# Kernel optimization log

Measured on AMD Instinct MI355X. Metric: run time of the kernel, lower is better.

## Reference

```python
import jax, jax.numpy as jnp
import numpy as np

N = 50000      # nodes
E = 600000     # edges (avg degree 12)
F_IN = 128     # num_features
H = 128        # hidden_feats (== F_IN so both conv layers share weight shapes)
C = 10         # num_classes
L = 2          # num_layers


def setup_inputs() -> dict:
    key = jax.random.key(0)
    ks = jax.random.split(key, 12)
    s = 0.05
    x = jax.random.normal(ks[0], (N, F_IN), dtype=jnp.float32)
    edge_index = jax.random.randint(ks[1], (2, E), 0, N, dtype=jnp.int64)
    # Stacked per-layer TransformerConv params (heads=1): query/key/value/skip linears.
    Wq = jax.random.normal(ks[2], (L, H, F_IN), dtype=jnp.float32) * s
    bq = jax.random.normal(ks[3], (L, H), dtype=jnp.float32) * s
    Wk = jax.random.normal(ks[4], (L, H, F_IN), dtype=jnp.float32) * s
    bk = jax.random.normal(ks[5], (L, H), dtype=jnp.float32) * s
    Wv = jax.random.normal(ks[6], (L, H, F_IN), dtype=jnp.float32) * s
    bv = jax.random.normal(ks[7], (L, H), dtype=jnp.float32) * s
    Ws = jax.random.normal(ks[8], (L, H, F_IN), dtype=jnp.float32) * s
    bs = jax.random.normal(ks[9], (L, H), dtype=jnp.float32) * s
    fc_W = jax.random.normal(ks[10], (C, H), dtype=jnp.float32) * s
    fc_b = jax.random.normal(ks[11], (C,), dtype=jnp.float32) * s
    return {"x": x, "edge_index": edge_index, "Wq": Wq, "bq": bq, "Wk": Wk,
            "bk": bk, "Wv": Wv, "bv": bv, "Ws": Ws, "bs": bs,
            "fc_W": fc_W, "fc_b": fc_b}


def _transformer_conv(h, src, dst, Wq, bq, Wk, bk, Wv, bv, Ws, bs):
    # PyG TransformerConv, heads=1, concat=True, root_weight=True, eval mode.
    d = Wq.shape[0]
    scale = 1.0 / np.sqrt(d).astype(np.float32)
    q = h @ Wq.T + bq          # [N, d]
    k = h @ Wk.T + bk          # [N, d]
    v = h @ Wv.T + bv          # [N, d]
    # per-edge attention score: <q_dst, k_src> / sqrt(d)
    scores = jnp.sum(q[dst] * k[src], axis=-1) * scale   # [E]
    # scatter-softmax over incoming edges of each destination node
    m = jax.ops.segment_max(scores, dst, num_segments=N)           # [N]
    e = jnp.exp(scores - m[dst])                                   # [E]
    denom = jax.ops.segment_sum(e, dst, num_segments=N)            # [N]
    alpha = e / denom[dst]                                         # [E]
    agg = jax.ops.segment_sum(alpha[:, None] * v[src], dst, num_segments=N)  # [N, d]
    return agg + (h @ Ws.T + bs)  # root/skip connection


def reference(x, edge_index, Wq, bq, Wk, bk, Wv, bv, Ws, bs, fc_W, fc_b):
    src = edge_index[0]
    dst = edge_index[1]
    h = x
    for l in range(L):  # fixed small layer loop
        h = _transformer_conv(h, src, dst, Wq[l], bq[l], Wk[l], bk[l],
                              Wv[l], bv[l], Ws[l], bs[l])
        h = jax.nn.relu(h)  # dropout is identity in eval mode
    logits = h @ fc_W.T + fc_b  # [N, C]
    return jax.nn.log_softmax(logits, axis=1)
```

## Files before the change

### kernel.cpp

```cpp
#include <hip/hip_runtime.h>
#include <math.h>

#define N_NODES 50000
#define N_EDGES 600000
#define DIM 128
#define NCLS 10
#define MTILES 391
#define CHUNKS_PER_TILE 2048
#define NB_SCAN 49

typedef __attribute__((ext_vector_type(8))) short short8b;
typedef __attribute__((ext_vector_type(4))) float f32x4;

__device__ inline unsigned short f2b(float f) {
    unsigned u = __float_as_uint(f);
    return (unsigned short)((u + 0x7FFFu + ((u >> 16) & 1u)) >> 16);
}
__device__ inline float b2f(unsigned short u) {
    return __uint_as_float(((unsigned)u) << 16);
}

__global__ void deg_kernel(const int* __restrict__ dst, int* __restrict__ deg) {
    int e = blockIdx.x * blockDim.x + threadIdx.x;
    if (e < N_EDGES) atomicAdd(&deg[dst[e]], 1);
}

__global__ __launch_bounds__(1024) void scan1_kernel(
        const int* __restrict__ deg, int* __restrict__ row_start,
        int* __restrict__ partials) {
    __shared__ int buf[1024];
    int b = blockIdx.x, t = threadIdx.x;
    int i = b * 1024 + t;
    buf[t] = (i < N_NODES) ? deg[i] : 0;
    __syncthreads();
    for (int off = 1; off < 1024; off <<= 1) {
        int tv = (t >= off) ? buf[t - off] : 0;
        __syncthreads();
        buf[t] += tv;
        __syncthreads();
    }
    if (i < N_NODES) row_start[i + 1] = buf[t];
    if (t == 1023) partials[b] = buf[1023];
}

__global__ void scan2_kernel(const int* __restrict__ partials, int* __restrict__ blockoff) {
    if (threadIdx.x == 0) {
        int off = 0;
        for (int b = 0; b < NB_SCAN; ++b) { blockoff[b] = off; off += partials[b]; }
    }
}

__global__ __launch_bounds__(1024) void scan3_kernel(
        const int* __restrict__ blockoff, int* __restrict__ row_start) {
    int b = blockIdx.x, t = threadIdx.x;
    int i = b * 1024 + t;
    if (i < N_NODES) row_start[i + 1] += blockoff[b];
    if (i == 0) row_start[0] = 0;
}

__global__ void fill_kernel(const int* __restrict__ src, const int* __restrict__ dst,
                            const int* __restrict__ row_start, int* __restrict__ cursor,
                            int* __restrict__ col) {
    int e = blockIdx.x * blockDim.x + threadIdx.x;
    if (e < N_EDGES) {
        int d = dst[e];
        int pos = atomicAdd(&cursor[d], 1);
        col[row_start[d] + pos] = src[e];
    }
}

__global__ __launch_bounds__(256) void wfrag_kernel(
        const float* __restrict__ Wq, const float* __restrict__ Wk,
        const float* __restrict__ Wv, const float* __restrict__ Ws,
        short* __restrict__ wfrag) {
    int mat = blockIdx.x;
    int l = mat >> 2, m = mat & 3;
    const float* W = (m == 0 ? Wq : m == 1 ? Wk : m == 2 ? Wv : Ws) + l * DIM * DIM;
    short* out = wfrag + (size_t)mat * (CHUNKS_PER_TILE * 8);
    for (int i = threadIdx.x; i < CHUNKS_PER_TILE; i += 256) {
        int tile = i >> 6, lane = i & 63;
        int row = (tile >> 2) * 16 + (lane & 15);
        int k0 = (tile & 3) * 32 + (lane >> 4) * 8;
        const float4* p = (const float4*)(W + row * DIM + k0);
        float4 a = p[0], b = p[1];
        short tmp[8];
        tmp[0] = (short)f2b(a.x); tmp[1] = (short)f2b(a.y);
        tmp[2] = (short)f2b(a.z); tmp[3] = (short)f2b(a.w);
        tmp[4] = (short)f2b(b.x); tmp[5] = (short)f2b(b.y);
        tmp[6] = (short)f2b(b.z); tmp[7] = (short)f2b(b.w);
        *(short8b*)(out + (size_t)i * 8) = *(short8b*)tmp;
    }
}

__global__ __launch_bounds__(256) void xb_kernel(const float* __restrict__ x,
                                                 unsigned short* __restrict__ xb) {
    int i = blockIdx.x * 256 + threadIdx.x;
    if (i >= N_NODES * DIM / 8) return;
    const float4* p = (const float4*)(x + (size_t)i * 8);
    float4 a = p[0], b = p[1];
    unsigned short tmp[8];
    tmp[0] = f2b(a.x); tmp[1] = f2b(a.y); tmp[2] = f2b(a.z); tmp[3] = f2b(a.w);
    tmp[4] = f2b(b.x); tmp[5] = f2b(b.y); tmp[6] = f2b(b.z); tmp[7] = f2b(b.w);
    *(short8b*)(xb + (size_t)i * 8) = *(short8b*)tmp;
}

__global__ __launch_bounds__(512) void linear_kernel(
        const unsigned short* __restrict__ hb,
        const short* __restrict__ wfrag,
        const float* __restrict__ bq, const float* __restrict__ bk,
        const float* __restrict__ bv, const float* __restrict__ bs,
        unsigned short* __restrict__ Qb, unsigned short* __restrict__ Kb,
        unsigned short* __restrict__ Vb, unsigned short* __restrict__ Sb) {
    __shared__ short hs[16384];
    __shared__ short wsm[16384];
    int tid = threadIdx.x;
    int tile = blockIdx.x;
    short8b* lh = (short8b*)hs;
    short8b* lw = (short8b*)wsm;
    #pragma unroll
    for (int j = 0; j < 4; ++j) {
        int i = tid + j * 512;
        int s = i >> 6, lane = i & 63;
        int row = tile * 128 + ((s >> 2) << 4) + (lane & 15);
        int k0 = ((s & 3) << 5) + ((lane >> 4) << 3);
        row = row < N_NODES ? row : N_NODES - 1;
        lh[i] = *(const short8b*)((const short*)hb + (size_t)row * DIM + k0);
    }
    int wave = tid >> 6, lane = tid & 63;
    int colg = lane & 15, rowg = lane >> 4;

    for (int m = 0; m < 4; ++m) {
        const short8b* gw = (const short8b*)(wfrag + (size_t)m * (CHUNKS_PER_TILE * 8));
        __syncthreads();
        #pragma unroll
        for (int j = 0; j < 4; ++j) lw[tid + j * 512] = gw[tid + j * 512];
        __syncthreads();

        f32x4 acc[8];
        #pragma unroll
        for (int nt = 0; nt < 8; ++nt) acc[nt] = (f32x4){0.f, 0.f, 0.f, 0.f};
        #pragma unroll
        for (int ks = 0; ks < 4; ++ks) {
            short8b a = lh[(wave * 4 + ks) * 64 + lane];
            #pragma unroll
            for (int nt = 0; nt < 8; ++nt)
                acc[nt] = __builtin_amdgcn_mfma_f32_16x16x32_bf16(
                              a, lw[(nt * 4 + ks) * 64 + lane], acc[nt], 0, 0, 0);
        }

        const float* bias = (m == 0 ? bq : m == 1 ? bk : m == 2 ? bv : bs);
        unsigned short* out = (m == 0 ? Qb : m == 1 ? Kb : m == 2 ? Vb : Sb);
        int rowbase = tile * 128 + wave * 16 + rowg * 4;
        #pragma unroll
        for (int nt = 0; nt < 8; ++nt) {
            int colv = nt * 16 + colg;
            float bvv = bias[colv];
            #pragma unroll
            for (int r = 0; r < 4; ++r) {
                int row = rowbase + r;
                if (row < N_NODES)
                    out[(size_t)row * DIM + colv] = f2b(acc[nt][r] + bvv);
            }
        }
    }
}

__global__ __launch_bounds__(256) void attn_kernel(
        const unsigned short* __restrict__ Qb, const unsigned short* __restrict__ Kb,
        const unsigned short* __restrict__ Vb, const unsigned short* __restrict__ Sb,
        const int* __restrict__ row_start, const int* __restrict__ col,
        unsigned short* __restrict__ hout) {
    int wave = threadIdx.x >> 6;
    int lane = threadIdx.x & 63;
    int g = lane >> 4, gl = lane & 15;
    int n = blockIdx.x * 4 + wave;
    if (n >= N_NODES) return;

    short8b qu = *(const short8b*)((const short*)Qb + (size_t)n * DIM + gl * 8);
    float qf[8];
    #pragma unroll
    for (int j = 0; j < 8; ++j) qf[j] = b2f((unsigned short)qu[j]);

    int e0 = row_start[n], e1 = row_start[n + 1];
    const float NEG = -1.0e30f;
    float m = NEG, den = 0.f;
    float acc[8];
    #pragma unroll
    for (int j = 0; j < 8; ++j) acc[j] = 0.f;
    const float scale = 0.08838834764831843f;

    for (int eb = e0; eb < e1; eb += 4) {
        int e = eb + g;
        bool valid = e < e1;
        int s = col[valid ? e : e1 - 1];
        const short* base = (const short*)Kb + (size_t)s * DIM + gl * 8;
        short8b kv = *(const short8b*)base;
        short8b vv = *(const short8b*)((const short*)Vb + (size_t)s * DIM + gl * 8);
        float p = 0.f;
        #pragma unroll
        for (int j = 0; j < 8; ++j) p = fmaf(qf[j], b2f((unsigned short)kv[j]), p);
        p += __shfl_xor(p, 1);
        p += __shfl_xor(p, 2);
        p += __shfl_xor(p, 4);
        p += __shfl_xor(p, 8);
        p = valid ? p * scale : NEG;
        float nm = fmaxf(m, p);
        float fac = __expf(m - nm);
        float w = valid ? __expf(p - nm) : 0.f;
        den = den * fac + w;
        #pragma unroll
        for (int j = 0; j < 8; ++j)
            acc[j] = fmaf(acc[j], fac, w * b2f((unsigned short)vv[j]));
        m = nm;
    }

    float M = m;
    M = fmaxf(M, __shfl_xor(M, 16));
    M = fmaxf(M, __shfl_xor(M, 32));
    float fac = __expf(m - M);
    float d = den * fac;
    d += __shfl_xor(d, 16);
    d += __shfl_xor(d, 32);
    #pragma unroll
    for (int j = 0; j < 8; ++j) {
        float a = acc[j] * fac;
        a += __shfl_xor(a, 16);
        a += __shfl_xor(a, 32);
        acc[j] = a;
    }
    float inv = (d > 0.f) ? 1.f / d : 0.f;

    short8b su = *(const short8b*)((const short*)Sb + (size_t)n * DIM + gl * 8);
    short8b o;
    #pragma unroll
    for (int j = 0; j < 8; ++j)
        o[j] = (short)f2b(fmaxf(fmaf(acc[j], inv, b2f((unsigned short)su[j])), 0.f));
    if (g == 0)
        *(short8b*)((short*)hout + (size_t)n * DIM + gl * 8) = o;
}

__global__ __launch_bounds__(256) void logits_kernel(
        const unsigned short* __restrict__ hb, const float* __restrict__ fcW,
        const float* __restrict__ fcb, float* __restrict__ out) {
    int wave = threadIdx.x >> 6, lane = threadIdx.x & 63;
    int n = blockIdx.x * 4 + wave;
    if (n >= N_NODES) return;
    ushort2 hu = ((const ushort2*)hb)[(size_t)n * 64 + lane];
    float hx = b2f(hu.x), hy = b2f(hu.y);
    float logit[NCLS];
    #pragma unroll
    for (int c = 0; c < NCLS; ++c) {
        float2 w = ((const float2*)(fcW + c * DIM))[lane];
        float p = hx * w.x + hy * w.y;
        #pragma unroll
        for (int off = 32; off >= 1; off >>= 1) p += __shfl_xor(p, off);
        logit[c] = p + fcb[c];
    }
    float mx = logit[0];
    #pragma unroll
    for (int c = 1; c < NCLS; ++c) mx = fmaxf(mx, logit[c]);
    float se = 0.f;
    #pragma unroll
    for (int c = 0; c < NCLS; ++c) se += __expf(logit[c] - mx);
    float lse = mx + logf(se);
    if (lane < NCLS) {
        float myv = 0.f;
        #pragma unroll
        for (int c = 0; c < NCLS; ++c) if (lane == c) myv = logit[c];
        out[(size_t)n * NCLS + lane] = myv - lse;
    }
}

extern "C" void kernel_launch(void* const* d_in, const int* in_sizes, int n_in,
                              void* d_out, int out_size, void* d_ws, size_t ws_size,
                              hipStream_t stream) {
    const float* x   = (const float*)d_in[0];
    const int*   ei  = (const int*)d_in[1];
    const float* Wq  = (const float*)d_in[2];
    const float* bq  = (const float*)d_in[3];
    const float* Wk  = (const float*)d_in[4];
    const float* bk  = (const float*)d_in[5];
    const float* Wv  = (const float*)d_in[6];
    const float* bv  = (const float*)d_in[7];
    const float* Ws  = (const float*)d_in[8];
    const float* bs  = (const float*)d_in[9];
    const float* fcW = (const float*)d_in[10];
    const float* fcb = (const float*)d_in[11];
    const int* src = ei;
    const int* dst = ei + N_EDGES;

    size_t NF = (size_t)N_NODES * DIM;
    unsigned short* Qb = (unsigned short*)d_ws;
    unsigned short* Kb = Qb + NF;
    unsigned short* Vb = Kb + NF;
    unsigned short* Sb = Vb + NF;
    unsigned short* h1 = Sb + NF;
    unsigned short* xb = h1 + NF;
    short* wfrag = (short*)(xb + NF);
    int* ints      = (int*)(wfrag + 8 * CHUNKS_PER_TILE * 8);
    int* row_start = ints;
    int* cursor    = row_start + N_NODES + 1;
    int* col       = cursor + N_NODES;
    int* partials  = col + N_EDGES;
    int* blockoff  = partials + 64;

    hipMemsetAsync(cursor, 0, N_NODES * sizeof(int), stream);
    deg_kernel<<<(N_EDGES + 255) / 256, 256, 0, stream>>>(dst, cursor);
    scan1_kernel<<<NB_SCAN, 1024, 0, stream>>>(cursor, row_start, partials);
    scan2_kernel<<<1, 64, 0, stream>>>(partials, blockoff);
    scan3_kernel<<<NB_SCAN, 1024, 0, stream>>>(blockoff, row_start);
    hipMemsetAsync(cursor, 0, N_NODES * sizeof(int), stream);
    fill_kernel<<<(N_EDGES + 255) / 256, 256, 0, stream>>>(src, dst, row_start, cursor, col);

    wfrag_kernel<<<8, 256, 0, stream>>>(Wq, Wk, Wv, Ws, wfrag);
    xb_kernel<<<(N_NODES * DIM / 8 + 255) / 256, 256, 0, stream>>>(x, xb);

    const int AGRID = (N_NODES + 3) / 4;

    linear_kernel<<<MTILES, 512, 0, stream>>>(xb, wfrag, bq, bk, bv, bs, Qb, Kb, Vb, Sb);
    attn_kernel<<<AGRID, 256, 0, stream>>>(Qb, Kb, Vb, Sb, row_start, col, h1);
    linear_kernel<<<MTILES, 512, 0, stream>>>(h1, wfrag + 4 * CHUNKS_PER_TILE * 8,
                                              bq + DIM, bk + DIM, bv + DIM, bs + DIM,
                                              Qb, Kb, Vb, Sb);
    attn_kernel<<<AGRID, 256, 0, stream>>>(Qb, Kb, Vb, Sb, row_start, col, xb);
    logits_kernel<<<AGRID, 256, 0, stream>>>(xb, fcW, fcb, (float*)d_out);
}
```

Before: 282.0 us.

## Trim launches, vectorize linear epilogue, streamline attention inner loop

```diff
diff --git a/kernel.cpp b/kernel.cpp
--- a/kernel.cpp
+++ b/kernel.cpp
@@ -8,6 +8,7 @@
 #define MTILES 391
 #define CHUNKS_PER_TILE 2048
 #define NB_SCAN 49
+#define XB_CHUNKS (N_NODES * DIM / 8)
 
 typedef __attribute__((ext_vector_type(8))) short short8b;
 typedef __attribute__((ext_vector_type(4))) float f32x4;
@@ -16,9 +17,14 @@
     unsigned u = __float_as_uint(f);
     return (unsigned short)((u + 0x7FFFu + ((u >> 16) & 1u)) >> 16);
 }
+__device__ inline unsigned pk2(float a, float b) {
+    return (unsigned)f2b(a) | ((unsigned)f2b(b) << 16);
+}
 __device__ inline float b2f(unsigned short u) {
     return __uint_as_float(((unsigned)u) << 16);
 }
+__device__ inline float blo(unsigned u) { return __uint_as_float(u << 16); }
+__device__ inline float bhi(unsigned u) { return __uint_as_float(u & 0xFFFF0000u); }
 
 __global__ void deg_kernel(const int* __restrict__ dst, int* __restrict__ deg) {
     int e = blockIdx.x * blockDim.x + threadIdx.x;
@@ -44,64 +50,72 @@
 }
 
 __global__ void scan2_kernel(const int* __restrict__ partials, int* __restrict__ blockoff) {
-    if (threadIdx.x == 0) {
-        int off = 0;
-        for (int b = 0; b < NB_SCAN; ++b) { blockoff[b] = off; off += partials[b]; }
-    }
+    int l = threadIdx.x;
+    int v = (l < NB_SCAN) ? partials[l] : 0;
+    int inc = v;
+    #pragma unroll
+    for (int off = 1; off < 64; off <<= 1) {
+        int t = __shfl_up(inc, off);
+        if (l >= off) inc += t;
+    }
+    if (l < NB_SCAN) blockoff[l] = inc - v;
 }
 
 __global__ __launch_bounds__(1024) void scan3_kernel(
-        const int* __restrict__ blockoff, int* __restrict__ row_start) {
+        const int* __restrict__ blockoff, int* __restrict__ row_start,
+        int* __restrict__ cursor) {
     int b = blockIdx.x, t = threadIdx.x;
     int i = b * 1024 + t;
-    if (i < N_NODES) row_start[i + 1] += blockoff[b];
-    if (i == 0) row_start[0] = 0;
+    if (i < N_NODES) {
+        int val = row_start[i + 1] + blockoff[b];
+        row_start[i + 1] = val;
+        if (i + 1 < N_NODES) cursor[i + 1] = val;
+    }
+    if (i == 0) { row_start[0] = 0; cursor[0] = 0; }
 }
 
 __global__ void fill_kernel(const int* __restrict__ src, const int* __restrict__ dst,
-                            const int* __restrict__ row_start, int* __restrict__ cursor,
-                            int* __restrict__ col) {
+                            int* __restrict__ cursor, int* __restrict__ col) {
     int e = blockIdx.x * blockDim.x + threadIdx.x;
     if (e < N_EDGES) {
-        int d = dst[e];
-        int pos = atomicAdd(&cursor[d], 1);
-        col[row_start[d] + pos] = src[e];
-    }
-}
-
-__global__ __launch_bounds__(256) void wfrag_kernel(
+        int pos = atomicAdd(&cursor[dst[e]], 1);
+        col[pos] = src[e];
+    }
+}
+
+__global__ __launch_bounds__(256) void convert_kernel(
+        const float* __restrict__ x,
         const float* __restrict__ Wq, const float* __restrict__ Wk,
         const float* __restrict__ Wv, const float* __restrict__ Ws,
-        short* __restrict__ wfrag) {
-    int mat = blockIdx.x;
-    int l = mat >> 2, m = mat & 3;
-    const float* W = (m == 0 ? Wq : m == 1 ? Wk : m == 2 ? Wv : Ws) + l * DIM * DIM;
-    short* out = wfrag + (size_t)mat * (CHUNKS_PER_TILE * 8);
-    for (int i = threadIdx.x; i < CHUNKS_PER_TILE; i += 256) {
-        int tile = i >> 6, lane = i & 63;
-        int row = (tile >> 2) * 16 + (lane & 15);
-        int k0 = (tile & 3) * 32 + (lane >> 4) * 8;
-        const float4* p = (const float4*)(W + row * DIM + k0);
-        float4 a = p[0], b = p[1];
-        short tmp[8];
-        tmp[0] = (short)f2b(a.x); tmp[1] = (short)f2b(a.y);
-        tmp[2] = (short)f2b(a.z); tmp[3] = (short)f2b(a.w);
-        tmp[4] = (short)f2b(b.x); tmp[5] = (short)f2b(b.y);
-        tmp[6] = (short)f2b(b.z); tmp[7] = (short)f2b(b.w);
-        *(short8b*)(out + (size_t)i * 8) = *(short8b*)tmp;
-    }
-}
-
-__global__ __launch_bounds__(256) void xb_kernel(const float* __restrict__ x,
-                                                 unsigned short* __restrict__ xb) {
-    int i = blockIdx.x * 256 + threadIdx.x;
-    if (i >= N_NODES * DIM / 8) return;
-    const float4* p = (const float4*)(x + (size_t)i * 8);
-    float4 a = p[0], b = p[1];
-    unsigned short tmp[8];
-    tmp[0] = f2b(a.x); tmp[1] = f2b(a.y); tmp[2] = f2b(a.z); tmp[3] = f2b(a.w);
-    tmp[4] = f2b(b.x); tmp[5] = f2b(b.y); tmp[6] = f2b(b.z); tmp[7] = f2b(b.w);
-    *(short8b*)(xb + (size_t)i * 8) = *(short8b*)tmp;
+        unsigned short* __restrict__ xb, short* __restrict__ wfrag) {
+    int b = blockIdx.x;
+    if (b < 8) {
+        int l = b >> 2, m = b & 3;
+        const float* W = (m == 0 ? Wq : m == 1 ? Wk : m == 2 ? Wv : Ws) + l * DIM * DIM;
+        short* out = wfrag + (size_t)b * (CHUNKS_PER_TILE * 8);
+        for (int i = threadIdx.x; i < CHUNKS_PER_TILE; i += 256) {
+            int tile = i >> 6, lane = i & 63;
+            int row = (tile >> 2) * 16 + (lane & 15);
+            int k0 = (tile & 3) * 32 + (lane >> 4) * 8;
+            const float4* p = (const float4*)(W + row * DIM + k0);
+            float4 a = p[0], bb = p[1];
+            short tmp[8];
+            tmp[0] = (short)f2b(a.x);  tmp[1] = (short)f2b(a.y);
+            tmp[2] = (short)f2b(a.z);  tmp[3] = (short)f2b(a.w);
+            tmp[4] = (short)f2b(bb.x); tmp[5] = (short)f2b(bb.y);
+            tmp[6] = (short)f2b(bb.z); tmp[7] = (short)f2b(bb.w);
+            *(short8b*)(out + (size_t)i * 8) = *(short8b*)tmp;
+        }
+    } else {
+        int i = (b - 8) * 256 + threadIdx.x;
+        if (i >= XB_CHUNKS) return;
+        const float4* p = (const float4*)(x + (size_t)i * 8);
+        float4 a = p[0], bb = p[1];
+        unsigned r0 = pk2(a.x, a.y), r1 = pk2(a.z, a.w);
+        unsigned r2 = pk2(bb.x, bb.y), r3 = pk2(bb.z, bb.w);
+        uint4 o = make_uint4(r0, r1, r2, r3);
+        *(uint4*)(xb + (size_t)i * 8) = o;
+    }
 }
 
 __global__ __launch_bounds__(512) void linear_kernel(
@@ -127,7 +141,8 @@
         lh[i] = *(const short8b*)((const short*)hb + (size_t)row * DIM + k0);
     }
     int wave = tid >> 6, lane = tid & 63;
-    int colg = lane & 15, rowg = lane >> 4;
+    int node = tile * 128 + wave * 16 + (lane & 15);
+    int cq = (lane >> 4) * 4;
 
     for (int m = 0; m < 4; ++m) {
         const short8b* gw = (const short8b*)(wfrag + (size_t)m * (CHUNKS_PER_TILE * 8));
@@ -141,25 +156,24 @@
         for (int nt = 0; nt < 8; ++nt) acc[nt] = (f32x4){0.f, 0.f, 0.f, 0.f};
         #pragma unroll
         for (int ks = 0; ks < 4; ++ks) {
-            short8b a = lh[(wave * 4 + ks) * 64 + lane];
+            short8b hbv = lh[(wave * 4 + ks) * 64 + lane];
             #pragma unroll
             for (int nt = 0; nt < 8; ++nt)
                 acc[nt] = __builtin_amdgcn_mfma_f32_16x16x32_bf16(
-                              a, lw[(nt * 4 + ks) * 64 + lane], acc[nt], 0, 0, 0);
+                              lw[(nt * 4 + ks) * 64 + lane], hbv, acc[nt], 0, 0, 0);
         }
 
         const float* bias = (m == 0 ? bq : m == 1 ? bk : m == 2 ? bv : bs);
         unsigned short* out = (m == 0 ? Qb : m == 1 ? Kb : m == 2 ? Vb : Sb);
-        int rowbase = tile * 128 + wave * 16 + rowg * 4;
-        #pragma unroll
-        for (int nt = 0; nt < 8; ++nt) {
-            int colv = nt * 16 + colg;
-            float bvv = bias[colv];
+        if (node < N_NODES) {
             #pragma unroll
-            for (int r = 0; r < 4; ++r) {
-                int row = rowbase + r;
-                if (row < N_NODES)
-                    out[(size_t)row * DIM + colv] = f2b(acc[nt][r] + bvv);
+            for (int nt = 0; nt < 8; ++nt) {
+                int colv = nt * 16 + cq;
+                float4 bi = *(const float4*)(bias + colv);
+                uint2 o;
+                o.x = pk2(acc[nt][0] + bi.x, acc[nt][1] + bi.y);
+                o.y = pk2(acc[nt][2] + bi.z, acc[nt][3] + bi.w);
+                *(uint2*)(out + (size_t)node * DIM + colv) = o;
             }
         }
     }
@@ -176,48 +190,93 @@
     int n = blockIdx.x * 4 + wave;
     if (n >= N_NODES) return;
 
-    short8b qu = *(const short8b*)((const short*)Qb + (size_t)n * DIM + gl * 8);
-    float qf[8];
-    #pragma unroll
-    for (int j = 0; j < 8; ++j) qf[j] = b2f((unsigned short)qu[j]);
+    const char* Kc = (const char*)Kb;
+    const char* Vc = (const char*)Vb;
+    const float qs = 0.08838834764831843f * 1.4426950408889634f;
+    uint4 qu = *(const uint4*)((const char*)Qb + (((unsigned)n) << 8) + (gl << 4));
+    float q0 = blo(qu.x) * qs, q1 = bhi(qu.x) * qs;
+    float q2 = blo(qu.y) * qs, q3 = bhi(qu.y) * qs;
+    float q4 = blo(qu.z) * qs, q5 = bhi(qu.z) * qs;
+    float q6 = blo(qu.w) * qs, q7 = bhi(qu.w) * qs;
 
     int e0 = row_start[n], e1 = row_start[n + 1];
+    int eq_end = e0 + ((e1 - e0) & ~3);
     const float NEG = -1.0e30f;
     float m = NEG, den = 0.f;
     float acc[8];
     #pragma unroll
     for (int j = 0; j < 8; ++j) acc[j] = 0.f;
-    const float scale = 0.08838834764831843f;
-
-    for (int eb = e0; eb < e1; eb += 4) {
-        int e = eb + g;
-        bool valid = e < e1;
-        int s = col[valid ? e : e1 - 1];
-        const short* base = (const short*)Kb + (size_t)s * DIM + gl * 8;
-        short8b kv = *(const short8b*)base;
-        short8b vv = *(const short8b*)((const short*)Vb + (size_t)s * DIM + gl * 8);
-        float p = 0.f;
-        #pragma unroll
-        for (int j = 0; j < 8; ++j) p = fmaf(qf[j], b2f((unsigned short)kv[j]), p);
+
+    int e = e0 + g;
+    for (; e < eq_end; e += 4) {
+        int s = col[e];
+        unsigned off = (((unsigned)s) << 8) + (gl << 4);
+        uint4 kv = *(const uint4*)(Kc + off);
+        uint4 vv = *(const uint4*)(Vc + off);
+        float p;
+        p = blo(kv.x) * q0;
+        p = fmaf(bhi(kv.x), q1, p);
+        p = fmaf(blo(kv.y), q2, p);
+        p = fmaf(bhi(kv.y), q3, p);
+        p = fmaf(blo(kv.z), q4, p);
+        p = fmaf(bhi(kv.z), q5, p);
+        p = fmaf(blo(kv.w), q6, p);
+        p = fmaf(bhi(kv.w), q7, p);
         p += __shfl_xor(p, 1);
         p += __shfl_xor(p, 2);
         p += __shfl_xor(p, 4);
         p += __shfl_xor(p, 8);
-        p = valid ? p * scale : NEG;
         float nm = fmaxf(m, p);
-        float fac = __expf(m - nm);
-        float w = valid ? __expf(p - nm) : 0.f;
-        den = den * fac + w;
-        #pragma unroll
-        for (int j = 0; j < 8; ++j)
-            acc[j] = fmaf(acc[j], fac, w * b2f((unsigned short)vv[j]));
+        float fac = exp2f(m - nm);
+        float w = exp2f(p - nm);
+        den = fmaf(den, fac, w);
+        acc[0] = fmaf(acc[0], fac, w * blo(vv.x));
+        acc[1] = fmaf(acc[1], fac, w * bhi(vv.x));
+        acc[2] = fmaf(acc[2], fac, w * blo(vv.y));
+        acc[3] = fmaf(acc[3], fac, w * bhi(vv.y));
+        acc[4] = fmaf(acc[4], fac, w * blo(vv.z));
+        acc[5] = fmaf(acc[5], fac, w * bhi(vv.z));
+        acc[6] = fmaf(acc[6], fac, w * blo(vv.w));
+        acc[7] = fmaf(acc[7], fac, w * bhi(vv.w));
+        m = nm;
+    }
+    if (e < e1) {
+        int s = col[e];
+        unsigned off = (((unsigned)s) << 8) + (gl << 4);
+        uint4 kv = *(const uint4*)(Kc + off);
+        uint4 vv = *(const uint4*)(Vc + off);
+        float p;
+        p = blo(kv.x) * q0;
+        p = fmaf(bhi(kv.x), q1, p);
+        p = fmaf(blo(kv.y), q2, p);
+        p = fmaf(bhi(kv.y), q3, p);
+        p = fmaf(blo(kv.z), q4, p);
+        p = fmaf(bhi(kv.z), q5, p);
+        p = fmaf(blo(kv.w), q6, p);
+        p = fmaf(bhi(kv.w), q7, p);
+        p += __shfl_xor(p, 1);
+        p += __shfl_xor(p, 2);
+        p += __shfl_xor(p, 4);
+        p += __shfl_xor(p, 8);
+        float nm = fmaxf(m, p);
+        float fac = exp2f(m - nm);
+        float w = exp2f(p - nm);
+        den = fmaf(den, fac, w);
+        acc[0] = fmaf(acc[0], fac, w * blo(vv.x));
+        acc[1] = fmaf(acc[1], fac, w * bhi(vv.x));
+        acc[2] = fmaf(acc[2], fac, w * blo(vv.y));
+        acc[3] = fmaf(acc[3], fac, w * bhi(vv.y));
+        acc[4] = fmaf(acc[4], fac, w * blo(vv.z));
+        acc[5] = fmaf(acc[5], fac, w * bhi(vv.z));
+        acc[6] = fmaf(acc[6], fac, w * blo(vv.w));
+        acc[7] = fmaf(acc[7], fac, w * bhi(vv.w));
         m = nm;
     }
 
     float M = m;
     M = fmaxf(M, __shfl_xor(M, 16));
     M = fmaxf(M, __shfl_xor(M, 32));
-    float fac = __expf(m - M);
+    float fac = exp2f(m - M);
     float d = den * fac;
     d += __shfl_xor(d, 16);
     d += __shfl_xor(d, 32);
@@ -230,13 +289,19 @@
     }
     float inv = (d > 0.f) ? 1.f / d : 0.f;
 
-    short8b su = *(const short8b*)((const short*)Sb + (size_t)n * DIM + gl * 8);
-    short8b o;
-    #pragma unroll
-    for (int j = 0; j < 8; ++j)
-        o[j] = (short)f2b(fmaxf(fmaf(acc[j], inv, b2f((unsigned short)su[j])), 0.f));
-    if (g == 0)
-        *(short8b*)((short*)hout + (size_t)n * DIM + gl * 8) = o;
+    uint4 su = *(const uint4*)((const char*)Sb + (((unsigned)n) << 8) + (gl << 4));
+    if (g == 0) {
+        uint4 o;
+        o.x = pk2(fmaxf(fmaf(acc[0], inv, blo(su.x)), 0.f),
+                  fmaxf(fmaf(acc[1], inv, bhi(su.x)), 0.f));
+        o.y = pk2(fmaxf(fmaf(acc[2], inv, blo(su.y)), 0.f),
+                  fmaxf(fmaf(acc[3], inv, bhi(su.y)), 0.f));
+        o.z = pk2(fmaxf(fmaf(acc[4], inv, blo(su.z)), 0.f),
+                  fmaxf(fmaf(acc[5], inv, bhi(su.z)), 0.f));
+        o.w = pk2(fmaxf(fmaf(acc[6], inv, blo(su.w)), 0.f),
+                  fmaxf(fmaf(acc[7], inv, bhi(su.w)), 0.f));
+        *(uint4*)((char*)hout + (((unsigned)n) << 8) + (gl << 4)) = o;
+    }
 }
 
 __global__ __launch_bounds__(256) void logits_kernel(
@@ -308,12 +373,11 @@
     deg_kernel<<<(N_EDGES + 255) / 256, 256, 0, stream>>>(dst, cursor);
     scan1_kernel<<<NB_SCAN, 1024, 0, stream>>>(cursor, row_start, partials);
     scan2_kernel<<<1, 64, 0, stream>>>(partials, blockoff);
-    scan3_kernel<<<NB_SCAN, 1024, 0, stream>>>(blockoff, row_start);
-    hipMemsetAsync(cursor, 0, N_NODES * sizeof(int), stream);
-    fill_kernel<<<(N_EDGES + 255) / 256, 256, 0, stream>>>(src, dst, row_start, cursor, col);
-
-    wfrag_kernel<<<8, 256, 0, stream>>>(Wq, Wk, Wv, Ws, wfrag);
-    xb_kernel<<<(N_NODES * DIM / 8 + 255) / 256, 256, 0, stream>>>(x, xb);
+    scan3_kernel<<<NB_SCAN, 1024, 0, stream>>>(blockoff, row_start, cursor);
+    fill_kernel<<<(N_EDGES + 255) / 256, 256, 0, stream>>>(src, dst, cursor, col);
+
+    convert_kernel<<<8 + (XB_CHUNKS + 255) / 256, 256, 0, stream>>>(
+        x, Wq, Wk, Wv, Ws, xb, wfrag);
 
     const int AGRID = (N_NODES + 3) / 4;
 
```

Result: faster. 273.8 us (-2.9%).
